# Optimization experiments

Hardware: AMD Instinct MI355X
Metric: run time of the kernel (lower is better)

## Reference

```python
import jax, jax.numpy as jnp
import numpy as np

NGROUP, CIN, COUT, K, HIDDEN = 8, 16, 16, 5, True


def _build_mask():
    # Group-causal PixelCNN-style mask for a 5x5 kernel.
    # Spatial: rows above center fully visible; center row visible left of center.
    # Center tap: input group g_in visible to output group g_out iff
    #   g_in <= g_out (hidden layer) or g_in < g_out (input layer).
    nout, cinall = NGROUP * COUT, NGROUP * CIN
    c = K // 2
    m = np.zeros((nout, cinall, K, K), dtype=np.float32)
    m[:, :, :c, :] = 1.0          # rows strictly above center
    m[:, :, c, :c] = 1.0          # center row, left of center
    g_out = np.arange(nout)[:, None] // COUT   # (nout,1)
    g_in = np.arange(cinall)[None, :] // CIN   # (1,cinall)
    center_ok = (g_in <= g_out) if HIDDEN else (g_in < g_out)
    m[:, :, c, c] = center_ok.astype(np.float32)
    return jnp.asarray(m)

_MASK = _build_mask()


def setup_inputs() -> dict:
    key = jax.random.key(0)
    k1, k2 = jax.random.split(key)
    x = jax.random.normal(k1, (8, 128, 256, 512), dtype=jnp.float32)
    weight = jax.random.uniform(k2, (128, 128, 5, 5), dtype=jnp.float32)
    bias = jnp.zeros((128,), dtype=jnp.float32)
    slope = jnp.zeros((128,), dtype=jnp.float32)  # PReLU slope (zero -> ReLU)
    return {"x": x, "weight": weight, "bias": bias, "slope": slope}


def reference(x, weight, bias, slope):
    w = weight * _MASK  # apply causal group mask
    # context pad by 2 then valid 5x5 conv == SAME padding conv
    y = jax.lax.conv_general_dilated(
        x, w, window_strides=(1, 1), padding=((2, 2), (2, 2)),
        dimension_numbers=("NCHW", "OIHW", "NCHW"))
    y = y + bias[None, :, None, None]
    a = slope[None, :, None, None]
    return jnp.where(y > 0, y, a * y)  # per-channel PReLU
```

## Files before the change

kernel.cpp:

```cpp
#include <hip/hip_runtime.h>
#include <hip/hip_bf16.h>

typedef __attribute__((ext_vector_type(8))) short short8;
typedef __attribute__((ext_vector_type(4))) float f32x4;

#define CH 128
#define H 256
#define W 512
#define PH 258
#define PW 516
#define NTAPS 13
#define P_BYTES (PH * PW * CH * 2)
#define P_SHORTS (PH * PW * CH)
#define CHW (CH * H * W)

#define GRAN_PER_ROW 544
#define NLOADS 52
#define BUF_SHORTS (3328 * 8)
#define ROW_SHORTS (GRAN_PER_ROW * 8)

#define GLD_LDS16(g, l)                                                        \
  __builtin_amdgcn_global_load_lds(                                            \
      (const __attribute__((address_space(1))) void*)(g),                      \
      (__attribute__((address_space(3))) void*)(l), 16, 0, 0)

__global__ void zero_pads(unsigned int* __restrict__ Pd) {
    int row  = blockIdx.x;
    int slab = blockIdx.y;
    unsigned int* base = Pd + (size_t)slab * (P_SHORTS / 2);
    int tid = threadIdx.x;
    if (row < 2) {
        unsigned int* r = base + (size_t)row * (PW * 64);
        for (int i = tid; i < PW * 64; i += 256) r[i] = 0u;
    } else {
        int seg = tid >> 6;
        int col = seg < 2 ? seg : 512 + seg;
        base[((size_t)row * PW + col) * 64 + (tid & 63)] = 0u;
    }
}

__global__ void premask_weights(const float* __restrict__ w,
                                __hip_bfloat16* __restrict__ Wt2) {
    int idx  = blockIdx.x * 256 + threadIdx.x;
    int frag = idx >> 9;
    int r    = idx & 511;
    int l    = r >> 3;
    int e    = r & 7;
    int t    = frag >> 5;
    int ob   = (frag >> 2) & 7;
    int kcg  = frag & 3;
    int oc   = ob * 16 + (l & 15);
    int ic   = kcg * 32 + (l >> 4) * 8 + e;
    int ky   = t < 5 ? 0 : (t < 10 ? 1 : 2);
    int kx   = t - ky * 5;
    float v  = w[(oc * CH + ic) * 25 + ky * 5 + kx];
    if (t == 12 && ((ic >> 4) > (oc >> 4))) v = 0.f;
    Wt2[idx] = __float2bfloat16(v);
}

__global__ void transpose_pad_all(const float* __restrict__ x,
                                  __hip_bfloat16* __restrict__ Pbase) {
    __shared__ float tile[32][33];
    const float* xn = x + (size_t)blockIdx.z * CHW;
    unsigned short* P = (unsigned short*)(Pbase + (size_t)blockIdx.z * P_SHORTS);
    int h  = blockIdx.y;
    int wt = blockIdx.x & 15;
    int ct = blockIdx.x >> 4;
    int tx = threadIdx.x & 31;
    int ty = threadIdx.x >> 5;
#pragma unroll
    for (int r = 0; r < 4; ++r) {
        int c = ct * 32 + ty + r * 8;
        tile[ty + r * 8][tx] = xn[(c * H + h) * W + wt * 32 + tx];
    }
    __syncthreads();
    int wl = threadIdx.x >> 3;
    int cq = threadIdx.x & 7;
    union { ushort4 u; __hip_bfloat16 hh[4]; } v;
    v.hh[0] = __float2bfloat16(tile[cq * 4 + 0][wl]);
    v.hh[1] = __float2bfloat16(tile[cq * 4 + 1][wl]);
    v.hh[2] = __float2bfloat16(tile[cq * 4 + 2][wl]);
    v.hh[3] = __float2bfloat16(tile[cq * 4 + 3][wl]);
    *reinterpret_cast<ushort4*>(
        P + ((size_t)(h + 2) * PW + (wt * 32 + wl + 2)) * CH + ct * 32 + cq * 4) = v.u;
}

__global__ __launch_bounds__(512, 2)
void conv_mfma_all(const __hip_bfloat16* __restrict__ Pbase,
                   const __hip_bfloat16* __restrict__ Wt2,
                   const float* __restrict__ bias,
                   const float* __restrict__ slope,
                   float* __restrict__ out) {
    __shared__ short ldsA[BUF_SHORTS];
    __shared__ short ldsB[BUF_SHORTS];
    const __hip_bfloat16* P = Pbase + (size_t)blockIdx.z * P_SHORTS;
    float* outn = out + (size_t)blockIdx.z * CHW;
    int h0    = blockIdx.y << 2;
    int w0    = blockIdx.x << 7;
    int tid   = threadIdx.x;
    int lane  = tid & 63;
    int wv    = tid >> 6;
    int l15   = lane & 15;
    int khi   = lane >> 4;
    int obf   = (wv & 1) * 4;
    int hsel  = wv >> 1;

    f32x4 acc[4][8];
#pragma unroll
    for (int mi = 0; mi < 4; ++mi)
#pragma unroll
        for (int ni = 0; ni < 8; ++ni)
            acc[mi][ni] = (f32x4){0.f, 0.f, 0.f, 0.f};

    const short* Wt2s = (const short*)Wt2;

    int stoff[7];
#pragma unroll
    for (int i = 0; i < 7; ++i) {
        int s    = wv + i * 8;
        int g64  = (s << 6) + lane;
        int row  = (g64 >= 544) + (g64 >= 1088) + (g64 >= 1632) +
                   (g64 >= 2176) + (g64 >= 2720) + (g64 >= 3264);
        int rowc = row < 6 ? row : 5;
        int G    = g64 - row * GRAN_PER_ROW;
        int pair = G >> 3;
        int qd   = (G & 7) ^ (pair & 7);
        int px   = pair * 2 + (qd >> 2);
        int chk  = qd & 3;
        int pxc  = px < 132 ? px : 131;
        stoff[i] = ((h0 + rowc) * PW + (w0 + pxc)) * CH + chk * 8;
    }
    int bq[5];
#pragma unroll
    for (int kx = 0; kx < 5; ++kx) {
        int pxb  = kx + l15;
        int pair = pxb >> 1;
        bq[kx] = ((pair << 3) + ((((pxb & 1) << 2) | khi) ^ (pair & 7))) << 3;
    }

    auto stage = [&](int kk, short* dst) {
#pragma unroll
        for (int i = 0; i < 7; ++i) {
            int s = wv + i * 8;
            if (s < NLOADS)
                GLD_LDS16(P + stoff[i] + kk * 32, (char*)dst + (s << 10));
        }
    };

    auto compute = [&](const short* __restrict__ bb0, int kk) {
        const short* apb = Wt2s + ((obf * 4 + kk) << 9) + (lane << 3);
        const short* bb  = bb0 + hsel * ROW_SHORTS;
#pragma unroll
        for (int t = 0; t < NTAPS; ++t) {
            int ky  = t < 5 ? 0 : (t < 10 ? 1 : 2);
            int kx  = t - ky * 5;
            const short* ap = apb + t * 16384;
            const short* bp = bb + ky * ROW_SHORTS + bq[kx];
            short8 a[4], b[8];
#pragma unroll
            for (int mi = 0; mi < 4; ++mi)
                a[mi] = *reinterpret_cast<const short8*>(ap + mi * 2048);
#pragma unroll
            for (int ni = 0; ni < 8; ++ni)
                b[ni] = *reinterpret_cast<const short8*>(bp + ni * 512);
            __builtin_amdgcn_s_setprio(1);
#pragma unroll
            for (int mi = 0; mi < 4; ++mi)
#pragma unroll
                for (int ni = 0; ni < 8; ++ni)
                    acc[mi][ni] = __builtin_amdgcn_mfma_f32_16x16x32_bf16(
                        a[mi], b[ni], acc[mi][ni], 0, 0, 0);
            __builtin_amdgcn_s_setprio(0);
        }
    };

    stage(0, ldsA);
    __syncthreads();

    stage(1, ldsB);
    compute(ldsA, 0);
    __syncthreads();

    stage(2, ldsA);
    compute(ldsB, 1);
    __syncthreads();

    stage(3, ldsB);
    compute(ldsA, 2);
    __syncthreads();

    compute(ldsB, 3);

    int hrow = h0 + hsel;
#pragma unroll
    for (int mi = 0; mi < 4; ++mi) {
        int ocb = obf * 16 + mi * 16 + 4 * khi;
        f32x4 b4 = *reinterpret_cast<const f32x4*>(bias + ocb);
        f32x4 s4 = *reinterpret_cast<const f32x4*>(slope + ocb);
#pragma unroll
        for (int i = 0; i < 4; ++i) {
            float* orow = outn + ((ocb + i) * H + hrow) * W + w0;
#pragma unroll
            for (int ni = 0; ni < 8; ++ni) {
                float v = acc[mi][ni][i] + b4[i];
                v = v > 0.f ? v : s4[i] * v;
                orow[ni * 16 + l15] = v;
            }
        }
    }
}

extern "C" void kernel_launch(void* const* d_in, const int* in_sizes, int n_in,
                              void* d_out, int out_size, void* d_ws, size_t ws_size,
                              hipStream_t stream) {
    const float* x      = (const float*)d_in[0];
    const float* weight = (const float*)d_in[1];
    const float* bias   = (const float*)d_in[2];
    const float* slope  = (const float*)d_in[3];
    float* out = (float*)d_out;

    __hip_bfloat16* Pbase = (__hip_bfloat16*)d_ws;
    __hip_bfloat16* Wt2   = (__hip_bfloat16*)((char*)d_ws + 8 * (size_t)P_BYTES);

    zero_pads<<<dim3(PH, 8), 256, 0, stream>>>((unsigned int*)d_ws);
    premask_weights<<<832, 256, 0, stream>>>(weight, Wt2);
    transpose_pad_all<<<dim3(64, 256, 8), 256, 0, stream>>>(x, Pbase);
    conv_mfma_all<<<dim3(4, 64, 8), 512, 0, stream>>>(Pbase, Wt2, bias, slope, out);
}
```

Before: 631.1 us.

## Software-pipeline weight loads and interleave LDS staging across taps

Restructures the conv main loop into a single unrolled k/tap loop that double-buffers the weight fragments in registers, prefetching the next tap's A operands while the current tap's MFMAs run. The global-to-LDS staging of the next channel chunk is spread over the first seven taps instead of issued as one burst. Two s_barriers per tap plus an explicit lgkmcnt wait and sched_barrier impose ordering. This aims to hide global weight-load latency and smooth memory traffic, at the cost of many extra workgroup barriers and more live registers.

```diff
diff --git a/kernel.cpp b/kernel.cpp
--- a/kernel.cpp
+++ b/kernel.cpp
@@ -91,8 +91,7 @@
                    const float* __restrict__ bias,
                    const float* __restrict__ slope,
                    float* __restrict__ out) {
-    __shared__ short ldsA[BUF_SHORTS];
-    __shared__ short ldsB[BUF_SHORTS];
+    __shared__ short lds[2 * BUF_SHORTS];
     const __hip_bfloat16* P = Pbase + (size_t)blockIdx.z * P_SHORTS;
     float* outn = out + (size_t)blockIdx.z * CHW;
     int h0    = blockIdx.y << 2;
@@ -138,58 +137,59 @@
         bq[kx] = ((pair << 3) + ((((pxb & 1) << 2) | khi) ^ (pair & 7))) << 3;
     }
 
-    auto stage = [&](int kk, short* dst) {
-#pragma unroll
-        for (int i = 0; i < 7; ++i) {
-            int s = wv + i * 8;
-            if (s < NLOADS)
-                GLD_LDS16(P + stoff[i] + kk * 32, (char*)dst + (s << 10));
-        }
+    short8 aA[4], aB[4];
+    auto aload = [&](short8* dst, int kk2, int t2) {
+        const short* ap = Wt2s + ((obf * 4 + kk2) << 9) + (lane << 3) + t2 * 16384;
+#pragma unroll
+        for (int mi = 0; mi < 4; ++mi)
+            dst[mi] = *reinterpret_cast<const short8*>(ap + mi * 2048);
     };
-
-    auto compute = [&](const short* __restrict__ bb0, int kk) {
-        const short* apb = Wt2s + ((obf * 4 + kk) << 9) + (lane << 3);
-        const short* bb  = bb0 + hsel * ROW_SHORTS;
+    auto stage1 = [&](int kk, int b, int i) {
+        int s = wv + i * 8;
+        if (s < NLOADS)
+            GLD_LDS16(P + stoff[i] + kk * 32,
+                      (char*)lds + b * (BUF_SHORTS * 2) + (s << 10));
+    };
+
+    aload(aA, 0, 0);
+#pragma unroll
+    for (int i = 0; i < 7; ++i) stage1(0, 0, i);
+    __syncthreads();
+
+#pragma unroll
+    for (int kk = 0; kk < 4; ++kk) {
+        const int cur = kk & 1;
+        const short* bb = lds + cur * BUF_SHORTS + hsel * ROW_SHORTS;
 #pragma unroll
         for (int t = 0; t < NTAPS; ++t) {
-            int ky  = t < 5 ? 0 : (t < 10 ? 1 : 2);
-            int kx  = t - ky * 5;
-            const short* ap = apb + t * 16384;
+            const int g  = kk * NTAPS + t;
+            short8* aU = (g & 1) ? aB : aA;
+            short8* aP = (g & 1) ? aA : aB;
+            const int ky = t < 5 ? 0 : (t < 10 ? 1 : 2);
+            const int kx = t - ky * 5;
             const short* bp = bb + ky * ROW_SHORTS + bq[kx];
-            short8 a[4], b[8];
-#pragma unroll
-            for (int mi = 0; mi < 4; ++mi)
-                a[mi] = *reinterpret_cast<const short8*>(ap + mi * 2048);
+            short8 b[8];
 #pragma unroll
             for (int ni = 0; ni < 8; ++ni)
                 b[ni] = *reinterpret_cast<const short8*>(bp + ni * 512);
+            if (t < 12)           aload(aP, kk, t + 1);
+            else if (kk < 3)      aload(aP, kk + 1, 0);
+            if (t < 7 && kk < 3)  stage1(kk + 1, cur ^ 1, t);
+            __builtin_amdgcn_s_barrier();
+            asm volatile("s_waitcnt lgkmcnt(0)" ::: "memory");
+            __builtin_amdgcn_sched_barrier(0);
             __builtin_amdgcn_s_setprio(1);
 #pragma unroll
             for (int mi = 0; mi < 4; ++mi)
 #pragma unroll
                 for (int ni = 0; ni < 8; ++ni)
                     acc[mi][ni] = __builtin_amdgcn_mfma_f32_16x16x32_bf16(
-                        a[mi], b[ni], acc[mi][ni], 0, 0, 0);
+                        aU[mi], b[ni], acc[mi][ni], 0, 0, 0);
             __builtin_amdgcn_s_setprio(0);
+            if (t == 12) __syncthreads();
+            else         __builtin_amdgcn_s_barrier();
         }
-    };
-
-    stage(0, ldsA);
-    __syncthreads();
-
-    stage(1, ldsB);
-    compute(ldsA, 0);
-    __syncthreads();
-
-    stage(2, ldsA);
-    compute(ldsB, 1);
-    __syncthreads();
-
-    stage(3, ldsB);
-    compute(ldsA, 2);
-    __syncthreads();
-
-    compute(ldsB, 3);
+    }
 
     int hrow = h0 + hsel;
 #pragma unroll
```

Result: slower. 703.8 us (+11.5%).
